# Kernel optimization log

Measured on AMD Instinct MI355X. Metric: run time of the kernel, lower is better.

The kernel has to match this reference:

```python
import jax, jax.numpy as jnp
import numpy as np

N = 50000   # nodes
C = 64      # channels (in == out)
E = 800000  # edges (before self-loops)
EPS = 1e-5  # BatchNorm eps


def _bn(h, gamma, beta):
    # training-mode BatchNorm1d over the node (batch) axis
    mu = h.mean(0)
    var = h.var(0)
    return (h - mu) * jax.lax.rsqrt(var + EPS) * gamma + beta


def setup_inputs() -> dict:
    key = jax.random.key(0)
    ks = jax.random.split(key, 20)
    p = lambda i, shape, s=0.1: jax.random.normal(ks[i], shape, jnp.float32) * s
    src = jax.random.randint(ks[2], (E,), 0, N, dtype=jnp.int32)
    # guarantee no self-loops (PointTransformerConv removes then re-adds them)
    dst = (src + 1 + jax.random.randint(ks[3], (E,), 0, N - 1, dtype=jnp.int32)) % N
    return dict(
        x=p(0, (N, C), 1.0),
        pos=p(1, (N, 3), 1.0),
        edge_index=jnp.stack([src, dst]),
        Win=p(4, (C, C)), bin_=p(5, (C,)), gin=jnp.ones((C,), jnp.float32), betain=jnp.zeros((C,), jnp.float32),
        Wv=p(6, (C, C)), Wk=p(7, (C, C)), Wq=p(8, (C, C)),
        P1=p(9, (3, C)), pb1=p(10, (C,)), P2=p(11, (C, C)), pb2=p(12, (C,)),
        A1=p(13, (C, C)), ab1=p(14, (C,)), A2=p(15, (C, C)), ab2=p(16, (C,)),
        Wout=p(17, (C, C)), bout=p(18, (C,)), gout=jnp.ones((C,), jnp.float32), betaout=jnp.zeros((C,), jnp.float32),
    )


def reference(x, pos, edge_index, Win, bin_, gin, betain, Wv, Wk, Wq,
              P1, pb1, P2, pb2, A1, ab1, A2, ab2, Wout, bout, gout, betaout):
    silu = jax.nn.silu
    # mlp_in: Linear + BN + SiLU (plain_last=False)
    x = silu(_bn(x @ Win + bin_, gin, betain))

    # PointTransformerConv (add_self_loops=True)
    loop = jnp.arange(N, dtype=edge_index.dtype)
    src = jnp.concatenate([edge_index[0], loop])  # j
    dst = jnp.concatenate([edge_index[1], loop])  # i

    v = x @ Wv       # lin (values), bias=False
    k = x @ Wk       # lin_src
    q = x @ Wq       # lin_dst

    # per-edge positional encoding: pos_nn = SiLU(SiLU((pos_i - pos_j) P1 + b) P2 + b)
    delta = silu(silu((pos[dst] - pos[src]) @ P1 + pb1) @ P2 + pb2)  # [Etot, C]
    # attention logits: attn_nn(alpha_i - alpha_j + delta)
    alpha = q[dst] - k[src] + delta
    alpha = silu(silu(alpha @ A1 + ab1) @ A2 + ab2)

    # segment-wise (per-dst-node, per-channel) softmax over neighborhoods
    m = jax.ops.segment_max(alpha, dst, num_segments=N)
    ex = jnp.exp(alpha - m[dst])
    denom = jax.ops.segment_sum(ex, dst, num_segments=N)
    attn = ex / denom[dst]

    # weighted scatter-reduce of messages
    out = jax.ops.segment_sum(attn * (v[src] + delta), dst, num_segments=N)  # [N, C]

    # mlp_out: Linear + BN, act=None
    return _bn(out @ Wout + bout, gout, betaout)
```

## Files before the change

kernel.cpp:

```cpp
#include <hip/hip_runtime.h>

#define CH 64
#define BN_EPS 1e-5f

typedef __attribute__((ext_vector_type(8))) __bf16 bf16x8;
typedef __attribute__((ext_vector_type(4))) float f32x4;

__device__ __forceinline__ float silu_f(float x) { return x / (1.0f + __expf(-x)); }

__global__ __launch_bounds__(256) void k_lin_in(
    const float* __restrict__ x, const float* __restrict__ Win, const float* __restrict__ bin,
    float* __restrict__ h, float* __restrict__ ssum, float* __restrict__ ssq, int N)
{
    __shared__ float xt[64 * 64];
    __shared__ float Wl[64 * 64];
    __shared__ float red[2][4][64];
    const int t = threadIdx.x, c = t & 63, g = t >> 6;
    const int row0 = blockIdx.x * 64;

    for (int i = t; i < 64 * 64; i += 256) {
        int r = i >> 6, cc = i & 63;
        int gr = row0 + r;
        xt[i] = (gr < N) ? x[(size_t)gr * CH + cc] : 0.0f;
        Wl[i] = Win[i];
    }
    __syncthreads();

    float acc[16];
    const float b = bin[c];
#pragma unroll
    for (int i = 0; i < 16; ++i) acc[i] = b;
    for (int k = 0; k < 64; ++k) {
        float w = Wl[k * 64 + c];
#pragma unroll
        for (int i = 0; i < 16; ++i) acc[i] += xt[(g * 16 + i) * 64 + k] * w;
    }
    float s = 0.0f, ss = 0.0f;
#pragma unroll
    for (int i = 0; i < 16; ++i) {
        int gr = row0 + g * 16 + i;
        if (gr < N) {
            h[(size_t)gr * CH + c] = acc[i];
            s += acc[i];
            ss += acc[i] * acc[i];
        }
    }
    red[0][g][c] = s;
    red[1][g][c] = ss;
    __syncthreads();
    if (g == 0) {
        atomicAdd(&ssum[c], red[0][0][c] + red[0][1][c] + red[0][2][c] + red[0][3][c]);
        atomicAdd(&ssq[c],  red[1][0][c] + red[1][1][c] + red[1][2][c] + red[1][3][c]);
    }
}

__global__ void k_stats(const float* __restrict__ ssum, const float* __restrict__ ssq,
                        const float* __restrict__ gamma, const float* __restrict__ beta,
                        float* __restrict__ scale, float* __restrict__ shift, int N)
{
    int c = threadIdx.x;
    float inv = 1.0f / (float)N;
    float mu = ssum[c] * inv;
    float var = ssq[c] * inv - mu * mu;
    float sc = gamma[c] * rsqrtf(var + BN_EPS);
    scale[c] = sc;
    shift[c] = beta[c] - mu * sc;
}

__global__ __launch_bounds__(256) void k_vkq(
    const float* __restrict__ h, const float* __restrict__ scale, const float* __restrict__ shift,
    const float* __restrict__ Wv, const float* __restrict__ Wk, const float* __restrict__ Wq,
    __bf16* __restrict__ vv, __bf16* __restrict__ kk, __bf16* __restrict__ qq, int N)
{
    __shared__ float xt[64 * 64];
    __shared__ float Wl[2][64 * 64];
    const int t = threadIdx.x, c = t & 63, g = t >> 6;
    const int row0 = blockIdx.x * 64;

    for (int i = t; i < 64 * 64; i += 256) {
        int r = i >> 6, cc = i & 63;
        int gr = row0 + r;
        float hv = (gr < N) ? h[(size_t)gr * CH + cc] : 0.0f;
        xt[i] = silu_f(hv * scale[cc] + shift[cc]);
        Wl[0][i] = Wv[i];
        Wl[1][i] = Wk[i];
    }
    __syncthreads();

    for (int m = 0; m < 2; ++m) {
        float acc[16];
#pragma unroll
        for (int i = 0; i < 16; ++i) acc[i] = 0.0f;
        for (int k = 0; k < 64; ++k) {
            float w = Wl[m][k * 64 + c];
#pragma unroll
            for (int i = 0; i < 16; ++i) acc[i] += xt[(g * 16 + i) * 64 + k] * w;
        }
        __bf16* o = (m == 0) ? vv : kk;
#pragma unroll
        for (int i = 0; i < 16; ++i) {
            int gr = row0 + g * 16 + i;
            if (gr < N) o[(size_t)gr * CH + c] = (__bf16)acc[i];
        }
    }
    __syncthreads();
    for (int i = t; i < 64 * 64; i += 256) Wl[0][i] = Wq[i];
    __syncthreads();
    {
        float acc[16];
#pragma unroll
        for (int i = 0; i < 16; ++i) acc[i] = 0.0f;
        for (int k = 0; k < 64; ++k) {
            float w = Wl[0][k * 64 + c];
#pragma unroll
            for (int i = 0; i < 16; ++i) acc[i] += xt[(g * 16 + i) * 64 + k] * w;
        }
#pragma unroll
        for (int i = 0; i < 16; ++i) {
            int gr = row0 + g * 16 + i;
            if (gr < N) qq[(size_t)gr * CH + c] = (__bf16)acc[i];
        }
    }
}

__global__ __launch_bounds__(256, 4) void k_edge_mfma(
    const int* __restrict__ srcA, const int* __restrict__ dstA,
    const float* __restrict__ pos,
    const __bf16* __restrict__ vvb, const __bf16* __restrict__ kkb, const __bf16* __restrict__ qqb,
    const float* __restrict__ P1, const float* __restrict__ pb1,
    const float* __restrict__ P2, const float* __restrict__ pb2,
    const float* __restrict__ A1, const float* __restrict__ ab1,
    const float* __restrict__ A2, const float* __restrict__ ab2,
    float* __restrict__ num, float* __restrict__ den,
    int E, int Etot, int nChunks)
{
    __shared__ __align__(16) __bf16 Wtab[3][8][64][8];
    __shared__ __align__(16) __bf16 tb[4][16][66];

    const int t = threadIdx.x;
    for (int i = t; i < 3 * 4096; i += 256) {
        int mat = i >> 12, r = i & 4095;
        int j = r & 7, lane = (r >> 3) & 63, ksnt = r >> 9;
        int ks = ksnt & 1, nt = ksnt >> 1;
        int k = ks * 32 + ((lane >> 4) & 3) * 8 + j;
        int n = nt * 16 + (lane & 15);
        const float* W = (mat == 0) ? P2 : ((mat == 1) ? A1 : A2);
        Wtab[mat][ksnt][lane][j] = (__bf16)W[k * 64 + n];
    }
    __syncthreads();

    const int l = t & 63, wid = t >> 6, lg = l >> 4, lm = l & 15;
    __bf16* tbw = &tb[wid][0][0];

    float pb1r[4], pb2r[4], ab1r[4], ab2r[4];
    bf16x8 p1f[4];
#pragma unroll
    for (int nt = 0; nt < 4; ++nt) {
        int co = nt * 16 + lm;
        pb1r[nt] = pb1[co]; pb2r[nt] = pb2[co];
        ab1r[nt] = ab1[co]; ab2r[nt] = ab2[co];
        bf16x8 f;
#pragma unroll
        for (int j = 0; j < 8; ++j)
            f[j] = (__bf16)((lg == 0 && j < 3) ? P1[j * 64 + co] : 0.0f);
        p1f[nt] = f;
    }

    const int stride = gridDim.x;
    int ch = blockIdx.x;
    if (ch >= nChunks) return;

    int sC = 0, dC = 0;
    {
        int eA = ch * 64 + wid * 16 + lm;
        if (eA < Etot) { if (eA < E) { sC = srcA[eA]; dC = dstA[eA]; } else { sC = dC = eA - E; } }
    }
    float pdl0, pdl1, pdl2;
    bf16x8 qmk0, qmk1;
    {
        const float* ps = pos + (size_t)sC * 3;
        const float* pd = pos + (size_t)dC * 3;
        pdl0 = pd[0] - ps[0]; pdl1 = pd[1] - ps[1]; pdl2 = pd[2] - ps[2];
        const __bf16* qp = qqb + (size_t)dC * 64 + lg * 8;
        const __bf16* kp = kkb + (size_t)sC * 64 + lg * 8;
        bf16x8 q0 = *(const bf16x8*)qp, q1 = *(const bf16x8*)(qp + 32);
        bf16x8 k0 = *(const bf16x8*)kp, k1 = *(const bf16x8*)(kp + 32);
#pragma unroll
        for (int j = 0; j < 8; ++j) {
            qmk0[j] = (__bf16)((float)q0[j] - (float)k0[j]);
            qmk1[j] = (__bf16)((float)q1[j] - (float)k1[j]);
        }
    }
    __bf16 vcur[4][4];
#pragma unroll
    for (int jj = 0; jj < 4; ++jj) {
        int sD = __shfl(sC, lg * 4 + jj);
        const __bf16* vp = vvb + (size_t)sD * 64 + lm;
#pragma unroll
        for (int nt = 0; nt < 4; ++nt) vcur[jj][nt] = vp[nt * 16];
    }
    int chn = ch + stride;
    bool hn = chn < nChunks;
    int sN = 0, dN = 0;
    if (hn) {
        int eA = chn * 64 + wid * 16 + lm;
        if (eA < Etot) { if (eA < E) { sN = srcA[eA]; dN = dstA[eA]; } else { sN = dN = eA - E; } }
    }

    for (;;) {
        const int e0 = ch * 64 + wid * 16;

        bf16x8 af;
        af[0] = (lg == 0) ? (__bf16)pdl0 : (__bf16)0.0f;
        af[1] = (lg == 0) ? (__bf16)pdl1 : (__bf16)0.0f;
        af[2] = (lg == 0) ? (__bf16)pdl2 : (__bf16)0.0f;
        af[3] = af[4] = af[5] = af[6] = af[7] = (__bf16)0.0f;
        f32x4 acc[4];
#pragma unroll
        for (int nt = 0; nt < 4; ++nt) {
            f32x4 a; a[0] = a[1] = a[2] = a[3] = pb1r[nt];
            acc[nt] = __builtin_amdgcn_mfma_f32_16x16x32_bf16(af, p1f[nt], a, 0, 0, 0);
        }
#pragma unroll
        for (int nt = 0; nt < 4; ++nt)
#pragma unroll
            for (int jj = 0; jj < 4; ++jj)
                tbw[(lg * 4 + jj) * 66 + nt * 16 + lm] = (__bf16)silu_f(acc[nt][jj]);
        bf16x8 aX0 = *(const bf16x8*)&tbw[lm * 66 + lg * 8];
        bf16x8 aX1 = *(const bf16x8*)&tbw[lm * 66 + 32 + lg * 8];

#pragma unroll
        for (int nt = 0; nt < 4; ++nt) {
            f32x4 a; a[0] = a[1] = a[2] = a[3] = pb2r[nt];
            a = __builtin_amdgcn_mfma_f32_16x16x32_bf16(aX0, *(const bf16x8*)&Wtab[0][nt * 2 + 0][l][0], a, 0, 0, 0);
            a = __builtin_amdgcn_mfma_f32_16x16x32_bf16(aX1, *(const bf16x8*)&Wtab[0][nt * 2 + 1][l][0], a, 0, 0, 0);
            acc[nt] = a;
        }
        float dlt[4][4];
#pragma unroll
        for (int nt = 0; nt < 4; ++nt)
#pragma unroll
            for (int jj = 0; jj < 4; ++jj) {
                float dv = silu_f(acc[nt][jj]);
                dlt[nt][jj] = dv;
                tbw[(lg * 4 + jj) * 66 + nt * 16 + lm] = (__bf16)dv;
            }

        float pdlN0, pdlN1, pdlN2;
        bf16x8 qmkN0, qmkN1;
        __bf16 vN[4][4];
        if (hn) {
            const float* ps = pos + (size_t)sN * 3;
            const float* pd = pos + (size_t)dN * 3;
            pdlN0 = pd[0] - ps[0]; pdlN1 = pd[1] - ps[1]; pdlN2 = pd[2] - ps[2];
            const __bf16* qp = qqb + (size_t)dN * 64 + lg * 8;
            const __bf16* kp = kkb + (size_t)sN * 64 + lg * 8;
            bf16x8 q0 = *(const bf16x8*)qp, q1 = *(const bf16x8*)(qp + 32);
            bf16x8 k0 = *(const bf16x8*)kp, k1 = *(const bf16x8*)(kp + 32);
#pragma unroll
            for (int j = 0; j < 8; ++j) {
                qmkN0[j] = (__bf16)((float)q0[j] - (float)k0[j]);
                qmkN1[j] = (__bf16)((float)q1[j] - (float)k1[j]);
            }
#pragma unroll
            for (int jj = 0; jj < 4; ++jj) {
                int sD = __shfl(sN, lg * 4 + jj);
                const __bf16* vp = vvb + (size_t)sD * 64 + lm;
#pragma unroll
                for (int nt = 0; nt < 4; ++nt) vN[jj][nt] = vp[nt * 16];
            }
        }

        const int chn2 = chn + stride;
        const bool hn2 = hn && (chn2 < nChunks);
        int sNN = 0, dNN = 0;
        if (hn2) {
            int eA = chn2 * 64 + wid * 16 + lm;
            if (eA < Etot) { if (eA < E) { sNN = srcA[eA]; dNN = dstA[eA]; } else { sNN = dNN = eA - E; } }
        }

        bf16x8 dA0 = *(const bf16x8*)&tbw[lm * 66 + lg * 8];
        bf16x8 dA1 = *(const bf16x8*)&tbw[lm * 66 + 32 + lg * 8];
        bf16x8 aA0, aA1;
#pragma unroll
        for (int j = 0; j < 8; ++j) {
            aA0[j] = (__bf16)((float)qmk0[j] + (float)dA0[j]);
            aA1[j] = (__bf16)((float)qmk1[j] + (float)dA1[j]);
        }

#pragma unroll
        for (int nt = 0; nt < 4; ++nt) {
            f32x4 a; a[0] = a[1] = a[2] = a[3] = ab1r[nt];
            a = __builtin_amdgcn_mfma_f32_16x16x32_bf16(aA0, *(const bf16x8*)&Wtab[1][nt * 2 + 0][l][0], a, 0, 0, 0);
            a = __builtin_amdgcn_mfma_f32_16x16x32_bf16(aA1, *(const bf16x8*)&Wtab[1][nt * 2 + 1][l][0], a, 0, 0, 0);
            acc[nt] = a;
        }
#pragma unroll
        for (int nt = 0; nt < 4; ++nt)
#pragma unroll
            for (int jj = 0; jj < 4; ++jj)
                tbw[(lg * 4 + jj) * 66 + nt * 16 + lm] = (__bf16)silu_f(acc[nt][jj]);
        bf16x8 aY0 = *(const bf16x8*)&tbw[lm * 66 + lg * 8];
        bf16x8 aY1 = *(const bf16x8*)&tbw[lm * 66 + 32 + lg * 8];

#pragma unroll
        for (int nt = 0; nt < 4; ++nt) {
            f32x4 a; a[0] = a[1] = a[2] = a[3] = ab2r[nt];
            a = __builtin_amdgcn_mfma_f32_16x16x32_bf16(aY0, *(const bf16x8*)&Wtab[2][nt * 2 + 0][l][0], a, 0, 0, 0);
            a = __builtin_amdgcn_mfma_f32_16x16x32_bf16(aY1, *(const bf16x8*)&Wtab[2][nt * 2 + 1][l][0], a, 0, 0, 0);
            acc[nt] = a;
        }

#pragma unroll
        for (int jj = 0; jj < 4; ++jj) {
            const int eD = e0 + lg * 4 + jj;
            const bool v = eD < Etot;
            const int dD = __shfl(dC, lg * 4 + jj);
            const size_t ob = (size_t)dD * 64 + lm;
#pragma unroll
            for (int nt = 0; nt < 4; ++nt) {
                float ex = v ? __expf(silu_f(acc[nt][jj])) : 0.0f;
                atomicAdd(&den[ob + nt * 16], ex);
                atomicAdd(&num[ob + nt * 16], ex * ((float)vcur[jj][nt] + dlt[nt][jj]));
            }
        }

        if (!hn) break;
        ch = chn; chn = chn2; hn = hn2;
        sC = sN; dC = dN; sN = sNN; dN = dNN;
        pdl0 = pdlN0; pdl1 = pdlN1; pdl2 = pdlN2;
        qmk0 = qmkN0; qmk1 = qmkN1;
#pragma unroll
        for (int jj = 0; jj < 4; ++jj)
#pragma unroll
            for (int nt = 0; nt < 4; ++nt) vcur[jj][nt] = vN[jj][nt];
    }
}

__global__ __launch_bounds__(256) void k_out(
    const float* __restrict__ num, const float* __restrict__ den,
    const float* __restrict__ Wout, const float* __restrict__ bout,
    float* __restrict__ o, float* __restrict__ ssum, float* __restrict__ ssq, int N)
{
    __shared__ float xt[64 * 64];
    __shared__ float Wl[64 * 64];
    __shared__ float red[2][4][64];
    const int t = threadIdx.x, c = t & 63, g = t >> 6;
    const int row0 = blockIdx.x * 64;

    for (int i = t; i < 64 * 64; i += 256) {
        int r = i >> 6, cc = i & 63;
        int gr = row0 + r;
        xt[i] = (gr < N) ? num[(size_t)gr * CH + cc] / den[(size_t)gr * CH + cc] : 0.0f;
        Wl[i] = Wout[i];
    }
    __syncthreads();

    float acc[16];
    const float b = bout[c];
#pragma unroll
    for (int i = 0; i < 16; ++i) acc[i] = b;
    for (int k = 0; k < 64; ++k) {
        float w = Wl[k * 64 + c];
#pragma unroll
        for (int i = 0; i < 16; ++i) acc[i] += xt[(g * 16 + i) * 64 + k] * w;
    }
    float s = 0.0f, ss = 0.0f;
#pragma unroll
    for (int i = 0; i < 16; ++i) {
        int gr = row0 + g * 16 + i;
        if (gr < N) {
            o[(size_t)gr * CH + c] = acc[i];
            s += acc[i];
            ss += acc[i] * acc[i];
        }
    }
    red[0][g][c] = s;
    red[1][g][c] = ss;
    __syncthreads();
    if (g == 0) {
        atomicAdd(&ssum[c], red[0][0][c] + red[0][1][c] + red[0][2][c] + red[0][3][c]);
        atomicAdd(&ssq[c],  red[1][0][c] + red[1][1][c] + red[1][2][c] + red[1][3][c]);
    }
}

__global__ void k_final(const float* __restrict__ o, const float* __restrict__ scale,
                        const float* __restrict__ shift, float* __restrict__ out, int total)
{
    int i = blockIdx.x * blockDim.x + threadIdx.x;
    if (i < total) {
        int c = i & 63;
        out[i] = o[i] * scale[c] + shift[c];
    }
}

extern "C" void kernel_launch(void* const* d_in, const int* in_sizes, int n_in,
                              void* d_out, int out_size, void* d_ws, size_t ws_size,
                              hipStream_t stream)
{
    const float* x      = (const float*)d_in[0];
    const float* pos    = (const float*)d_in[1];
    const int*   ei     = (const int*)d_in[2];
    const float* Win    = (const float*)d_in[3];
    const float* bin    = (const float*)d_in[4];
    const float* gin    = (const float*)d_in[5];
    const float* betain = (const float*)d_in[6];
    const float* Wv     = (const float*)d_in[7];
    const float* Wk     = (const float*)d_in[8];
    const float* Wq     = (const float*)d_in[9];
    const float* P1     = (const float*)d_in[10];
    const float* pb1    = (const float*)d_in[11];
    const float* P2     = (const float*)d_in[12];
    const float* pb2    = (const float*)d_in[13];
    const float* A1     = (const float*)d_in[14];
    const float* ab1    = (const float*)d_in[15];
    const float* A2     = (const float*)d_in[16];
    const float* ab2    = (const float*)d_in[17];
    const float* Wout   = (const float*)d_in[18];
    const float* bout   = (const float*)d_in[19];
    const float* gout   = (const float*)d_in[20];
    const float* betaout= (const float*)d_in[21];

    const int N = in_sizes[0] / CH;
    const int E = in_sizes[2] / 2;
    const int Etot = E + N;
    const int* srcA = ei;
    const int* dstA = ei + E;

    float* ws = (float*)d_ws;
    const size_t NC = (size_t)N * CH;
    float* h    = ws;
    float* num  = h + NC;
    float* den  = num + NC;
    float* st   = den + NC;
    __bf16* vvb = (__bf16*)(st + 512);
    __bf16* kkb = vvb + NC;
    __bf16* qqb = kkb + NC;

    hipMemsetAsync(num, 0, (2 * NC + 512) * sizeof(float), stream);

    const int nb = (N + 63) / 64;
    k_lin_in<<<nb, 256, 0, stream>>>(x, Win, bin, h, st, st + 64, N);
    k_stats<<<1, 64, 0, stream>>>(st, st + 64, gin, betain, st + 128, st + 192, N);
    k_vkq<<<nb, 256, 0, stream>>>(h, st + 128, st + 192, Wv, Wk, Wq, vvb, kkb, qqb, N);

    const int nChunks = (Etot + 63) / 64;
    const int grid = (nChunks < 1024) ? nChunks : 1024;
    k_edge_mfma<<<grid, 256, 0, stream>>>(srcA, dstA, pos, vvb, kkb, qqb,
                                          P1, pb1, P2, pb2, A1, ab1, A2, ab2,
                                          num, den, E, Etot, nChunks);

    k_out<<<nb, 256, 0, stream>>>(num, den, Wout, bout, h, st + 256, st + 320, N);
    k_stats<<<1, 64, 0, stream>>>(st + 256, st + 320, gout, betaout, st + 384, st + 448, N);
    k_final<<<(int)((NC + 255) / 256), 256, 0, stream>>>(h, st + 384, st + 448,
                                                         (float*)d_out, (int)NC);
}
```

Measured before the change: 580.1 us.

## Compute pos_nn first layer with VALU directly in MFMA A-operand layout

Replaces the K=3 MFMA for the first positional layer (padded to K=32) and its LDS round-trip with per-lane scalar FMAs. Each lane computes its A-fragment for the second layer directly, reading P1 and pb1 from shared memory. The delta values kept live until the scatter are stored as bf16 to save registers, and launch bounds drop from 4 to 2 waves per SIMD. The goal is to remove wasted MFMA work plus an LDS write/read and barrier-free shuffle per chunk, at the cost of extra VALU exp/div work, lower delta precision, and possibly lower occupancy.

```diff
diff --git a/kernel.cpp b/kernel.cpp
--- a/kernel.cpp
+++ b/kernel.cpp
@@ -4,6 +4,7 @@
 #define BN_EPS 1e-5f
 
 typedef __attribute__((ext_vector_type(8))) __bf16 bf16x8;
+typedef __attribute__((ext_vector_type(4))) __bf16 bf16x4;
 typedef __attribute__((ext_vector_type(4))) float f32x4;
 
 __device__ __forceinline__ float silu_f(float x) { return x / (1.0f + __expf(-x)); }
@@ -123,7 +124,7 @@
     }
 }
 
-__global__ __launch_bounds__(256, 4) void k_edge_mfma(
+__global__ __launch_bounds__(256, 2) void k_edge_mfma(
     const int* __restrict__ srcA, const int* __restrict__ dstA,
     const float* __restrict__ pos,
     const __bf16* __restrict__ vvb, const __bf16* __restrict__ kkb, const __bf16* __restrict__ qqb,
@@ -136,6 +137,8 @@
 {
     __shared__ __align__(16) __bf16 Wtab[3][8][64][8];
     __shared__ __align__(16) __bf16 tb[4][16][66];
+    __shared__ __align__(16) __bf16 P1L[3][64];
+    __shared__ __align__(16) float pb1L[64];
 
     const int t = threadIdx.x;
     for (int i = t; i < 3 * 4096; i += 256) {
@@ -147,23 +150,19 @@
         const float* W = (mat == 0) ? P2 : ((mat == 1) ? A1 : A2);
         Wtab[mat][ksnt][lane][j] = (__bf16)W[k * 64 + n];
     }
+    if (t < 192) P1L[t / 64][t & 63] = (__bf16)P1[t];
+    if (t < 64)  pb1L[t] = pb1[t];
     __syncthreads();
 
     const int l = t & 63, wid = t >> 6, lg = l >> 4, lm = l & 15;
     __bf16* tbw = &tb[wid][0][0];
 
-    float pb1r[4], pb2r[4], ab1r[4], ab2r[4];
-    bf16x8 p1f[4];
+    float pb2r[4], ab1r[4], ab2r[4];
 #pragma unroll
     for (int nt = 0; nt < 4; ++nt) {
         int co = nt * 16 + lm;
-        pb1r[nt] = pb1[co]; pb2r[nt] = pb2[co];
+        pb2r[nt] = pb2[co];
         ab1r[nt] = ab1[co]; ab2r[nt] = ab2[co];
-        bf16x8 f;
-#pragma unroll
-        for (int j = 0; j < 8; ++j)
-            f[j] = (__bf16)((lg == 0 && j < 3) ? P1[j * 64 + co] : 0.0f);
-        p1f[nt] = f;
     }
 
     const int stride = gridDim.x;
@@ -210,25 +209,25 @@
     for (;;) {
         const int e0 = ch * 64 + wid * 16;
 
-        bf16x8 af;
-        af[0] = (lg == 0) ? (__bf16)pdl0 : (__bf16)0.0f;
-        af[1] = (lg == 0) ? (__bf16)pdl1 : (__bf16)0.0f;
-        af[2] = (lg == 0) ? (__bf16)pdl2 : (__bf16)0.0f;
-        af[3] = af[4] = af[5] = af[6] = af[7] = (__bf16)0.0f;
+        bf16x8 aX0, aX1;
+#pragma unroll
+        for (int f = 0; f < 2; ++f) {
+            const int k0 = f * 32 + lg * 8;
+            bf16x8 w0 = *(const bf16x8*)&P1L[0][k0];
+            bf16x8 w1 = *(const bf16x8*)&P1L[1][k0];
+            bf16x8 w2 = *(const bf16x8*)&P1L[2][k0];
+            f32x4 b0 = *(const f32x4*)&pb1L[k0];
+            f32x4 b1 = *(const f32x4*)&pb1L[k0 + 4];
+#pragma unroll
+            for (int j = 0; j < 8; ++j) {
+                float bb = (j < 4) ? b0[j & 3] : b1[j & 3];
+                float tv = silu_f(pdl0 * (float)w0[j] + pdl1 * (float)w1[j] +
+                                  pdl2 * (float)w2[j] + bb);
+                if (f == 0) aX0[j] = (__bf16)tv; else aX1[j] = (__bf16)tv;
+            }
+        }
+
         f32x4 acc[4];
-#pragma unroll
-        for (int nt = 0; nt < 4; ++nt) {
-            f32x4 a; a[0] = a[1] = a[2] = a[3] = pb1r[nt];
-            acc[nt] = __builtin_amdgcn_mfma_f32_16x16x32_bf16(af, p1f[nt], a, 0, 0, 0);
-        }
-#pragma unroll
-        for (int nt = 0; nt < 4; ++nt)
-#pragma unroll
-            for (int jj = 0; jj < 4; ++jj)
-                tbw[(lg * 4 + jj) * 66 + nt * 16 + lm] = (__bf16)silu_f(acc[nt][jj]);
-        bf16x8 aX0 = *(const bf16x8*)&tbw[lm * 66 + lg * 8];
-        bf16x8 aX1 = *(const bf16x8*)&tbw[lm * 66 + 32 + lg * 8];
-
 #pragma unroll
         for (int nt = 0; nt < 4; ++nt) {
             f32x4 a; a[0] = a[1] = a[2] = a[3] = pb2r[nt];
@@ -236,17 +235,17 @@
             a = __builtin_amdgcn_mfma_f32_16x16x32_bf16(aX1, *(const bf16x8*)&Wtab[0][nt * 2 + 1][l][0], a, 0, 0, 0);
             acc[nt] = a;
         }
-        float dlt[4][4];
+        bf16x4 dltb[4];
 #pragma unroll
         for (int nt = 0; nt < 4; ++nt)
 #pragma unroll
             for (int jj = 0; jj < 4; ++jj) {
                 float dv = silu_f(acc[nt][jj]);
-                dlt[nt][jj] = dv;
+                dltb[nt][jj] = (__bf16)dv;
                 tbw[(lg * 4 + jj) * 66 + nt * 16 + lm] = (__bf16)dv;
             }
 
-        float pdlN0, pdlN1, pdlN2;
+        float pdlN0 = 0.f, pdlN1 = 0.f, pdlN2 = 0.f;
         bf16x8 qmkN0, qmkN1;
         __bf16 vN[4][4];
         if (hn) {
@@ -321,7 +320,7 @@
             for (int nt = 0; nt < 4; ++nt) {
                 float ex = v ? __expf(silu_f(acc[nt][jj])) : 0.0f;
                 atomicAdd(&den[ob + nt * 16], ex);
-                atomicAdd(&num[ob + nt * 16], ex * ((float)vcur[jj][nt] + dlt[nt][jj]));
+                atomicAdd(&num[ob + nt * 16], ex * ((float)vcur[jj][nt] + (float)dltb[nt][jj]));
             }
         }
 
```

After: 565.9 us. 2.4% less time.
